# Performance work log

Hardware: AMD Instinct MI355X
Metric: run time of the kernel (lower is better)

Reference implementation:

```python
import jax, jax.numpy as jnp
import numpy as np

B, W, F, N = 256, 512, 512, 512


def setup_inputs() -> dict:
    key = jax.random.key(0)
    k1, k2, k3, k4, k5 = jax.random.split(key, 5)
    return {
        "x": jax.random.normal(k1, (B, W, F), dtype=jnp.float32),
        "weight_k": jax.random.normal(k2, (F, N), dtype=jnp.float32),
        "weight_q": jax.random.normal(k3, (F, N), dtype=jnp.float32),
        "weight_v": jax.random.normal(k4, (F, N), dtype=jnp.float32),
        "w": jax.random.normal(k5, (W, 1), dtype=jnp.float32),
    }


def reference(x, weight_k, weight_q, weight_v, w):
    # x: (B, W, F)
    n_outputs = weight_k.shape[-1]
    # Per-word K/V projections (original loops over words; here one batched GEMM)
    K = jnp.einsum("bwf,fn->bwn", x, weight_k)  # (B, W, N)
    V = jnp.einsum("bwf,fn->bwn", x, weight_v)  # (B, W, N)
    # Per-sample query: t = x^T @ w -> (F,), q = t @ weight_q -> (N,)
    t = jnp.einsum("bwf,w->bf", x, w[:, 0])     # (B, F)
    Q = t @ weight_q                              # (B, N)
    # Scores over words, scaled, softmax across the word axis
    scores = jnp.einsum("bn,bwn->bw", Q, K) / jnp.sqrt(jnp.float32(n_outputs))
    weights = jax.nn.softmax(scores, axis=1)      # (B, W)
    # Weighted sum of V over words
    return jnp.einsum("bw,bwn->bn", weights, V)   # (B, N)
```

## Files before the change

kernel.cpp:

```cpp
#include <hip/hip_runtime.h>
#include <math.h>

#define B 256
#define W 512
#define F 512
#define N 512

__global__ __launch_bounds__(512) void prep_kernel(
    const float* __restrict__ x,
    const float* __restrict__ Wk,
    const float* __restrict__ Wq,
    const float* __restrict__ wvec,
    float* __restrict__ r_out)
{
    __shared__ float s_w[W];
    __shared__ float s_t[F];
    __shared__ float s_q[N];

    const int b   = blockIdx.x;
    const int tid = threadIdx.x;

    s_w[tid] = wvec[tid];
    __syncthreads();

    const float* xb = x + (size_t)b * W * F;
    float acc = 0.f;
#pragma unroll 8
    for (int w = 0; w < W; ++w) {
        acc += xb[(size_t)w * F + tid] * s_w[w];
    }
    s_t[tid] = acc;
    __syncthreads();

    float q = 0.f;
#pragma unroll 8
    for (int f = 0; f < F; ++f) {
        q += s_t[f] * Wq[(size_t)f * N + tid];
    }
    s_q[tid] = q;
    __syncthreads();

    const float4* wkrow = (const float4*)(Wk + (size_t)tid * N);
    float rv = 0.f;
#pragma unroll 4
    for (int n4 = 0; n4 < N / 4; ++n4) {
        float4 kv = wkrow[n4];
        float4 qv = *(const float4*)(&s_q[n4 * 4]);
        rv += kv.x * qv.x + kv.y * qv.y + kv.z * qv.z + kv.w * qv.w;
    }
    const float inv_sqrtN = 0.04419417382415922f;
    r_out[(size_t)b * F + tid] = rv * inv_sqrtN;
}

__global__ __launch_bounds__(512) void attn_kernel(
    const float* __restrict__ x,
    const float* __restrict__ Wv,
    const float* __restrict__ r_in,
    float* __restrict__ out)
{
    const int b    = blockIdx.x;
    const int tid  = threadIdx.x;
    const int lane = tid & 63;
    const int wv   = tid >> 6;

    __shared__ float s_c[8][F];
    __shared__ float s_m[8];
    __shared__ float s_l[8];
    __shared__ float s_cf[F];

    const float* xb = x + (size_t)b * W * F;
    const float* rb = r_in + (size_t)b * F;

    const float4 r0 = *(const float4*)(rb + lane * 4);
    const float4 r1 = *(const float4*)(rb + 256 + lane * 4);

    float m = -INFINITY;
    float l = 0.f;
    float4 c0 = make_float4(0.f, 0.f, 0.f, 0.f);
    float4 c1 = make_float4(0.f, 0.f, 0.f, 0.f);

#pragma unroll 2
    for (int i = 0; i < 64; ++i) {
        const int w = wv * 64 + i;
        const float* row = xb + (size_t)w * F;
        const float4 x0 = *(const float4*)(row + lane * 4);
        const float4 x1 = *(const float4*)(row + 256 + lane * 4);

        float d = x0.x * r0.x + x0.y * r0.y + x0.z * r0.z + x0.w * r0.w
                + x1.x * r1.x + x1.y * r1.y + x1.z * r1.z + x1.w * r1.w;
#pragma unroll
        for (int off = 32; off >= 1; off >>= 1) d += __shfl_xor(d, off, 64);

        const float mnew  = fmaxf(m, d);
        const float scale = __expf(m - mnew);
        const float p     = __expf(d - mnew);
        l = l * scale + p;
        c0.x = c0.x * scale + p * x0.x;
        c0.y = c0.y * scale + p * x0.y;
        c0.z = c0.z * scale + p * x0.z;
        c0.w = c0.w * scale + p * x0.w;
        c1.x = c1.x * scale + p * x1.x;
        c1.y = c1.y * scale + p * x1.y;
        c1.z = c1.z * scale + p * x1.z;
        c1.w = c1.w * scale + p * x1.w;
        m = mnew;
    }

    *(float4*)&s_c[wv][lane * 4]       = c0;
    *(float4*)&s_c[wv][256 + lane * 4] = c1;
    if (lane == 0) { s_m[wv] = m; s_l[wv] = l; }
    __syncthreads();

    float M = -INFINITY;
#pragma unroll
    for (int j = 0; j < 8; ++j) M = fmaxf(M, s_m[j]);
    float L = 0.f;
    float alpha[8];
#pragma unroll
    for (int j = 0; j < 8; ++j) {
        alpha[j] = __expf(s_m[j] - M);
        L += alpha[j] * s_l[j];
    }
    const float invL = 1.f / L;

    float cf = 0.f;
#pragma unroll
    for (int j = 0; j < 8; ++j) cf += alpha[j] * s_c[j][tid];
    s_cf[tid] = cf * invL;
    __syncthreads();

    float o = 0.f;
#pragma unroll 8
    for (int f = 0; f < F; ++f) {
        o += s_cf[f] * Wv[(size_t)f * N + tid];
    }
    out[(size_t)b * N + tid] = o;
}

extern "C" void kernel_launch(void* const* d_in, const int* in_sizes, int n_in,
                              void* d_out, int out_size, void* d_ws, size_t ws_size,
                              hipStream_t stream)
{
    const float* x    = (const float*)d_in[0];
    const float* Wk   = (const float*)d_in[1];
    const float* Wq   = (const float*)d_in[2];
    const float* Wv   = (const float*)d_in[3];
    const float* wvec = (const float*)d_in[4];
    float* out = (float*)d_out;
    float* r   = (float*)d_ws;

    prep_kernel<<<B, 512, 0, stream>>>(x, Wk, Wq, wvec, r);
    attn_kernel<<<B, 512, 0, stream>>>(x, Wv, r, out);
}
```

Baseline: 484.7 us.

## Split x^T w reduction across more blocks and add ILP to GEMV loops

The prep kernel is split in two. A new tpart kernel computes partial x^T·w sums over four word groups per sample using float4 loads, which gives four times as many blocks. A small qr kernel then sums the partials and computes q and r. The Q, Wk and Wv GEMV loops now use four independent accumulators, and the attention loop handles two rows per iteration to expose more memory and ILP parallelism. This adds a kernel launch and a workspace round-trip for the partial sums.

```diff
diff --git a/kernel.cpp b/kernel.cpp
--- a/kernel.cpp
+++ b/kernel.cpp
@@ -5,51 +5,83 @@
 #define W 512
 #define F 512
 #define N 512
-
-__global__ __launch_bounds__(512) void prep_kernel(
+#define GPART 4
+#define WPG (W / GPART)
+
+__global__ __launch_bounds__(512) void tpart_kernel(
     const float* __restrict__ x,
+    const float* __restrict__ wvec,
+    float* __restrict__ t_part)
+{
+    const int blk = blockIdx.x;
+    const int g   = blk & (GPART - 1);
+    const int b   = blk >> 2;
+    const int tid = threadIdx.x;
+    const int ws  = tid >> 7;
+    const int f4  = tid & 127;
+
+    __shared__ float s_w[WPG];
+    __shared__ float s_part[4][F];
+
+    if (tid < WPG) s_w[tid] = wvec[g * WPG + tid];
+    __syncthreads();
+
+    const float* xb = x + (size_t)b * W * F + (size_t)(g * WPG + ws * 32) * F;
+    float4 acc = make_float4(0.f, 0.f, 0.f, 0.f);
+#pragma unroll 8
+    for (int i = 0; i < 32; ++i) {
+        const float4 xv = *(const float4*)(xb + (size_t)i * F + f4 * 4);
+        const float  ww = s_w[ws * 32 + i];
+        acc.x += xv.x * ww; acc.y += xv.y * ww;
+        acc.z += xv.z * ww; acc.w += xv.w * ww;
+    }
+    *(float4*)&s_part[ws][f4 * 4] = acc;
+    __syncthreads();
+
+    const float t = (s_part[0][tid] + s_part[1][tid])
+                  + (s_part[2][tid] + s_part[3][tid]);
+    t_part[(size_t)blk * F + tid] = t;
+}
+
+__global__ __launch_bounds__(512) void qr_kernel(
+    const float* __restrict__ t_part,
+    const float* __restrict__ Wq,
     const float* __restrict__ Wk,
-    const float* __restrict__ Wq,
-    const float* __restrict__ wvec,
     float* __restrict__ r_out)
 {
-    __shared__ float s_w[W];
     __shared__ float s_t[F];
     __shared__ float s_q[N];
-
-    const int b   = blockIdx.x;
-    const int tid = threadIdx.x;
-
-    s_w[tid] = wvec[tid];
-    __syncthreads();
-
-    const float* xb = x + (size_t)b * W * F;
-    float acc = 0.f;
+    const int b = blockIdx.x, tid = threadIdx.x;
+
+    float t = 0.f;
+#pragma unroll
+    for (int g = 0; g < GPART; ++g)
+        t += t_part[((size_t)b * GPART + g) * F + tid];
+    s_t[tid] = t;
+    __syncthreads();
+
+    float q0 = 0.f, q1 = 0.f, q2 = 0.f, q3 = 0.f;
+#pragma unroll 4
+    for (int f = 0; f < F; f += 4) {
+        q0 += s_t[f + 0] * Wq[(size_t)(f + 0) * N + tid];
+        q1 += s_t[f + 1] * Wq[(size_t)(f + 1) * N + tid];
+        q2 += s_t[f + 2] * Wq[(size_t)(f + 2) * N + tid];
+        q3 += s_t[f + 3] * Wq[(size_t)(f + 3) * N + tid];
+    }
+    s_q[tid] = (q0 + q1) + (q2 + q3);
+    __syncthreads();
+
+    const float4* wkrow = (const float4*)(Wk + (size_t)tid * N);
+    float r0 = 0.f, r1 = 0.f, r2 = 0.f, r3 = 0.f;
 #pragma unroll 8
-    for (int w = 0; w < W; ++w) {
-        acc += xb[(size_t)w * F + tid] * s_w[w];
-    }
-    s_t[tid] = acc;
-    __syncthreads();
-
-    float q = 0.f;
-#pragma unroll 8
-    for (int f = 0; f < F; ++f) {
-        q += s_t[f] * Wq[(size_t)f * N + tid];
-    }
-    s_q[tid] = q;
-    __syncthreads();
-
-    const float4* wkrow = (const float4*)(Wk + (size_t)tid * N);
-    float rv = 0.f;
-#pragma unroll 4
     for (int n4 = 0; n4 < N / 4; ++n4) {
-        float4 kv = wkrow[n4];
-        float4 qv = *(const float4*)(&s_q[n4 * 4]);
-        rv += kv.x * qv.x + kv.y * qv.y + kv.z * qv.z + kv.w * qv.w;
-    }
-    const float inv_sqrtN = 0.04419417382415922f;
-    r_out[(size_t)b * F + tid] = rv * inv_sqrtN;
+        const float4 kv = wkrow[n4];
+        const float4 qv = *(const float4*)&s_q[n4 * 4];
+        r0 += kv.x * qv.x; r1 += kv.y * qv.y;
+        r2 += kv.z * qv.z; r3 += kv.w * qv.w;
+    }
+    r_out[(size_t)b * F + tid] =
+        ((r0 + r1) + (r2 + r3)) * 0.04419417382415922f;
 }
 
 __global__ __launch_bounds__(512) void attn_kernel(
@@ -70,40 +102,51 @@
 
     const float* xb = x + (size_t)b * W * F;
     const float* rb = r_in + (size_t)b * F;
-
     const float4 r0 = *(const float4*)(rb + lane * 4);
     const float4 r1 = *(const float4*)(rb + 256 + lane * 4);
 
-    float m = -INFINITY;
-    float l = 0.f;
+    float m = -INFINITY, l = 0.f;
     float4 c0 = make_float4(0.f, 0.f, 0.f, 0.f);
     float4 c1 = make_float4(0.f, 0.f, 0.f, 0.f);
 
 #pragma unroll 2
-    for (int i = 0; i < 64; ++i) {
-        const int w = wv * 64 + i;
-        const float* row = xb + (size_t)w * F;
-        const float4 x0 = *(const float4*)(row + lane * 4);
-        const float4 x1 = *(const float4*)(row + 256 + lane * 4);
-
-        float d = x0.x * r0.x + x0.y * r0.y + x0.z * r0.z + x0.w * r0.w
-                + x1.x * r1.x + x1.y * r1.y + x1.z * r1.z + x1.w * r1.w;
-#pragma unroll
-        for (int off = 32; off >= 1; off >>= 1) d += __shfl_xor(d, off, 64);
-
-        const float mnew  = fmaxf(m, d);
-        const float scale = __expf(m - mnew);
-        const float p     = __expf(d - mnew);
-        l = l * scale + p;
-        c0.x = c0.x * scale + p * x0.x;
-        c0.y = c0.y * scale + p * x0.y;
-        c0.z = c0.z * scale + p * x0.z;
-        c0.w = c0.w * scale + p * x0.w;
-        c1.x = c1.x * scale + p * x1.x;
-        c1.y = c1.y * scale + p * x1.y;
-        c1.z = c1.z * scale + p * x1.z;
-        c1.w = c1.w * scale + p * x1.w;
-        m = mnew;
+    for (int i = 0; i < 64; i += 2) {
+        const float* rowA = xb + (size_t)(wv * 64 + i) * F;
+        const float* rowB = rowA + F;
+        const float4 a0 = *(const float4*)(rowA + lane * 4);
+        const float4 a1 = *(const float4*)(rowA + 256 + lane * 4);
+        const float4 b0 = *(const float4*)(rowB + lane * 4);
+        const float4 b1 = *(const float4*)(rowB + 256 + lane * 4);
+
+        float dA = a0.x * r0.x + a0.y * r0.y + a0.z * r0.z + a0.w * r0.w
+                 + a1.x * r1.x + a1.y * r1.y + a1.z * r1.z + a1.w * r1.w;
+        float dB = b0.x * r0.x + b0.y * r0.y + b0.z * r0.z + b0.w * r0.w
+                 + b1.x * r1.x + b1.y * r1.y + b1.z * r1.z + b1.w * r1.w;
+#pragma unroll
+        for (int off = 32; off >= 1; off >>= 1) {
+            dA += __shfl_xor(dA, off, 64);
+            dB += __shfl_xor(dB, off, 64);
+        }
+
+        float mn = fmaxf(m, dA);
+        float sc = __expf(m - mn);
+        float p  = __expf(dA - mn);
+        l = l * sc + p;
+        c0.x = c0.x * sc + p * a0.x; c0.y = c0.y * sc + p * a0.y;
+        c0.z = c0.z * sc + p * a0.z; c0.w = c0.w * sc + p * a0.w;
+        c1.x = c1.x * sc + p * a1.x; c1.y = c1.y * sc + p * a1.y;
+        c1.z = c1.z * sc + p * a1.z; c1.w = c1.w * sc + p * a1.w;
+        m = mn;
+
+        mn = fmaxf(m, dB);
+        sc = __expf(m - mn);
+        p  = __expf(dB - mn);
+        l = l * sc + p;
+        c0.x = c0.x * sc + p * b0.x; c0.y = c0.y * sc + p * b0.y;
+        c0.z = c0.z * sc + p * b0.z; c0.w = c0.w * sc + p * b0.w;
+        c1.x = c1.x * sc + p * b1.x; c1.y = c1.y * sc + p * b1.y;
+        c1.z = c1.z * sc + p * b1.z; c1.w = c1.w * sc + p * b1.w;
+        m = mn;
     }
 
     *(float4*)&s_c[wv][lane * 4]       = c0;
@@ -129,12 +172,15 @@
     s_cf[tid] = cf * invL;
     __syncthreads();
 
-    float o = 0.f;
-#pragma unroll 8
-    for (int f = 0; f < F; ++f) {
-        o += s_cf[f] * Wv[(size_t)f * N + tid];
-    }
-    out[(size_t)b * N + tid] = o;
+    float o0 = 0.f, o1 = 0.f, o2 = 0.f, o3 = 0.f;
+#pragma unroll 4
+    for (int f = 0; f < F; f += 4) {
+        o0 += s_cf[f + 0] * Wv[(size_t)(f + 0) * N + tid];
+        o1 += s_cf[f + 1] * Wv[(size_t)(f + 1) * N + tid];
+        o2 += s_cf[f + 2] * Wv[(size_t)(f + 2) * N + tid];
+        o3 += s_cf[f + 3] * Wv[(size_t)(f + 3) * N + tid];
+    }
+    out[(size_t)b * N + tid] = (o0 + o1) + (o2 + o3);
 }
 
 extern "C" void kernel_launch(void* const* d_in, const int* in_sizes, int n_in,
@@ -146,9 +192,11 @@
     const float* Wq   = (const float*)d_in[2];
     const float* Wv   = (const float*)d_in[3];
     const float* wvec = (const float*)d_in[4];
-    float* out = (float*)d_out;
-    float* r   = (float*)d_ws;
-
-    prep_kernel<<<B, 512, 0, stream>>>(x, Wk, Wq, wvec, r);
+    float* out    = (float*)d_out;
+    float* t_part = (float*)d_ws;
+    float* r      = t_part + (size_t)B * GPART * F;
+
+    tpart_kernel<<<B * GPART, 512, 0, stream>>>(x, wvec, t_part);
+    qr_kernel<<<B, 512, 0, stream>>>(t_part, Wq, Wk, r);
     attn_kernel<<<B, 512, 0, stream>>>(x, Wv, r, out);
 }
```

After: 465.5 us. 1.04x faster.
